# Kernel tuning notes

Hardware: AMD Instinct MI355X
Metric: run time of the kernel (lower is better)

## Reference

```python
import jax, jax.numpy as jnp
import numpy as np

EMB = 2048
H = 16
Q_RANK = 1536
KV_RANK = 512
ROPE_D = 64
NOPE_D = 64
V_D = 128
QK_D = ROPE_D + NOPE_D  # 128
ROPE_BASE = 10000.0
SCALING = 1.0  # query_pre_attn_scalar ** -0.5 with scalar=1.0


def apply_rope(x):
    """torchtune-style interleaved RoPE. x: (B, S, H, D)."""
    S, D = x.shape[1], x.shape[-1]
    theta = 1.0 / (ROPE_BASE ** (jnp.arange(0, D, 2, dtype=jnp.float32) / D))  # (D/2,)
    ang = jnp.arange(S, dtype=jnp.float32)[:, None] * theta[None, :]  # (S, D/2)
    cos = jnp.cos(ang)[None, :, None, :]
    sin = jnp.sin(ang)[None, :, None, :]
    xf = x.astype(jnp.float32).reshape(*x.shape[:-1], D // 2, 2)
    x0, x1 = xf[..., 0], xf[..., 1]
    out = jnp.stack([x0 * cos - x1 * sin, x1 * cos + x0 * sin], axis=-1)
    return out.reshape(x.shape).astype(x.dtype)


def setup_inputs() -> dict:
    key = jax.random.key(0)
    ks = jax.random.split(key, 6)
    s = lambda fan_in: 1.0 / np.sqrt(fan_in)
    return {
        "x": jax.random.normal(ks[0], (2, 2048, EMB), dtype=jnp.float32),
        "q_a_w": jax.random.uniform(ks[1], (Q_RANK, EMB), jnp.float32, -s(EMB), s(EMB)),
        "q_b_w": jax.random.uniform(ks[2], (H * QK_D, Q_RANK), jnp.float32, -s(Q_RANK), s(Q_RANK)),
        "kv_a_w": jax.random.uniform(ks[3], (KV_RANK + ROPE_D, EMB), jnp.float32, -s(EMB), s(EMB)),
        "kv_b_w": jax.random.uniform(ks[4], (H * (NOPE_D + V_D), KV_RANK), jnp.float32, -s(KV_RANK), s(KV_RANK)),
        "o_w": jax.random.uniform(ks[5], (EMB, H * V_D), jnp.float32, -s(H * V_D), s(H * V_D)),
    }


def reference(x, q_a_w, q_b_w, kv_a_w, kv_b_w, o_w):
    B, S, _ = x.shape
    # LoRA-compressed Q projection
    q = (x @ q_a_w.T) @ q_b_w.T  # (B, S, H*QK_D)
    q = q.reshape(B, S, H, QK_D).transpose(0, 2, 1, 3)  # (B, H, S, QK_D)
    q_pass, q_rot = q[..., :NOPE_D], q[..., NOPE_D:]
    # Compressed KV with shared rope key
    ckv = x @ kv_a_w.T  # (B, S, KV_RANK + ROPE_D)
    k_pass_c, k_rot = ckv[..., :KV_RANK], ckv[..., KV_RANK:]
    kvb = (k_pass_c @ kv_b_w.T).reshape(B, S, H, NOPE_D + V_D).transpose(0, 2, 1, 3)
    k_pass, v = kvb[..., :NOPE_D], kvb[..., NOPE_D:]  # (B,H,S,NOPE_D), (B,H,S,V_D)
    # RoPE (applied in (B,S,H,D) layout, as in the original)
    q_rot = apply_rope(q_rot.transpose(0, 2, 1, 3)).transpose(0, 2, 1, 3)
    k_rot = apply_rope(k_rot[:, :, None, :])  # (B, S, 1, ROPE_D), shared across heads
    k_rot = jnp.broadcast_to(k_rot.transpose(0, 2, 1, 3), (B, H, S, ROPE_D))
    query = jnp.concatenate([q_pass, q_rot], axis=-1)  # (B, H, S, QK_D)
    key = jnp.concatenate([k_pass, k_rot], axis=-1)
    # NOTE: original passes attention_mask=None -> no causal mask applied.
    scores = jnp.einsum("bhqd,bhkd->bhqk", query, key) * SCALING
    attn = jax.nn.softmax(scores.astype(jnp.float32), axis=-1).astype(query.dtype)
    out = jnp.einsum("bhqk,bhkd->bhqd", attn, v)  # (B, H, S, V_D)
    out = out.transpose(0, 2, 1, 3).reshape(B, S, H * V_D)
    return out @ o_w.T
```

## Files before the change

### kernel.cpp

```cpp
#include <hip/hip_runtime.h>
#include <stdint.h>

#define EMB 2048
#define NH 16
#define QRANK 1536
#define KVRANK 512
#define ROPED 64
#define NOPED 64
#define VD 128
#define QKD 128
#define SEQ 2048
#define BATCH 2
#define BS 4096
#define BHD 32
#define NCOMB 2112
#define LOG2E 1.4426950408889634f
#define NT (SEQ / 64)

typedef __attribute__((ext_vector_type(4))) float f32x4;
typedef __attribute__((ext_vector_type(8))) short s16x8;
typedef __attribute__((ext_vector_type(4))) short s16x4;
typedef __attribute__((ext_vector_type(2))) unsigned int u32x2;

__device__ __forceinline__ float bf2f(unsigned short u) {
  return __uint_as_float(((unsigned int)u) << 16);
}
__device__ __forceinline__ unsigned short f2bf(float f) {
  unsigned int u = __float_as_uint(f);
  u += 0x7fff + ((u >> 16) & 1);
  return (unsigned short)(u >> 16);
}

__device__ __forceinline__ float vexp2(float x) {
#if __has_builtin(__builtin_amdgcn_exp2f)
  return __builtin_amdgcn_exp2f(x);
#else
  return exp2f(x);
#endif
}

__device__ __forceinline__ unsigned int pk_bf16_trunc(float e0, float e1) {
#if __has_builtin(__builtin_amdgcn_perm)
  return __builtin_amdgcn_perm(__float_as_uint(e1), __float_as_uint(e0), 0x07060302u);
#else
  return (__float_as_uint(e1) & 0xffff0000u) | (__float_as_uint(e0) >> 16);
#endif
}

__device__ __forceinline__ void pl32swap(unsigned int& a, unsigned int& b) {
#if __has_builtin(__builtin_amdgcn_permlane32_swap)
  u32x2 r = __builtin_amdgcn_permlane32_swap(a, b, false, false);
  a = r.x; b = r.y;
#else
  asm("v_permlane32_swap_b32 %0, %1" : "+v"(a), "+v"(b));
#endif
}
__device__ __forceinline__ void pl16swap(unsigned int& a, unsigned int& b) {
#if __has_builtin(__builtin_amdgcn_permlane16_swap)
  u32x2 r = __builtin_amdgcn_permlane16_swap(a, b, false, false);
  a = r.x; b = r.y;
#else
  asm("v_permlane16_swap_b32 %0, %1" : "+v"(a), "+v"(b));
#endif
}

__device__ __forceinline__ void gld_lds16(const unsigned short* g, unsigned short* l) {
  __builtin_amdgcn_global_load_lds((const __attribute__((address_space(1))) void*)g,
                                   (__attribute__((address_space(3))) void*)l,
                                   16, 0, 0);
}

#define N4_X   (BS * EMB / 4)
#define N4_QA  (QRANK * EMB / 4)
#define N4_KVA ((KVRANK + ROPED) * EMB / 4)
#define N4_QB  (NH * QKD * QRANK / 4)
#define N4_KVB (NH * 192 * KVRANK / 4)
#define N4_O   (EMB * NH * VD / 4)
#define N4_TOT (N4_X + N4_QA + N4_KVA + N4_QB + N4_KVB + N4_O)

__global__ void cast_all(const float* __restrict__ x, const float* __restrict__ qa,
                         const float* __restrict__ kva, const float* __restrict__ qb,
                         const float* __restrict__ kvb, const float* __restrict__ ow,
                         unsigned short* __restrict__ Xb, unsigned short* __restrict__ Wcomb,
                         unsigned short* __restrict__ Wqb, unsigned short* __restrict__ Wkvb,
                         unsigned short* __restrict__ Wo) {
  int i = blockIdx.x * blockDim.x + threadIdx.x;
  int stride = gridDim.x * blockDim.x;
  for (; i < N4_TOT; i += stride) {
    const float4* src;
    ushort4* dst;
    int j = i;
    if (j < N4_X) { src = (const float4*)x; dst = (ushort4*)Xb; }
    else if ((j -= N4_X) < N4_QA) { src = (const float4*)qa; dst = (ushort4*)Wcomb; }
    else if ((j -= N4_QA) < N4_KVA) { src = (const float4*)kva; dst = (ushort4*)(Wcomb + (size_t)QRANK * EMB); }
    else if ((j -= N4_KVA) < N4_QB) { src = (const float4*)qb; dst = (ushort4*)Wqb; }
    else if ((j -= N4_QB) < N4_KVB) { src = (const float4*)kvb; dst = (ushort4*)Wkvb; }
    else { j -= N4_KVB; src = (const float4*)ow; dst = (ushort4*)Wo; }
    float4 v = src[j];
    ushort4 o;
    o.x = f2bf(v.x); o.y = f2bf(v.y); o.z = f2bf(v.z); o.w = f2bf(v.w);
    dst[j] = o;
  }
}

template <int OUT_F32>
__global__ __launch_bounds__(256, 3) void gemm_bt(
    const unsigned short* __restrict__ A, int lda,
    const unsigned short* __restrict__ W, int ldw,
    void* __restrict__ C, int M, int N, int K)
{
  __shared__ __align__(16) unsigned short As[128 * 64];
  __shared__ __align__(16) unsigned short Ws[128 * 64];
  const int tid = threadIdx.x;
  const int wave = tid >> 6;
  const int lane = tid & 63;
  const int ln = lane & 15;
  const int quad = lane >> 4;
  const int nwg = gridDim.x;
  const int cpx = nwg >> 3;
  const int swz = (blockIdx.x & 7) * cpx + (blockIdx.x >> 3);
  const int nbx = (N + 127) >> 7;
  const int bm = (swz / nbx) * 128;
  const int bn = (swz % nbx) * 128;
  const int wm = (wave >> 1) * 64;
  const int wn = (wave & 1) * 64;

  f32x4 acc[4][4] = {};

  const int rel8 = lane >> 3;
  const int csw = ((lane & 7) ^ rel8) * 8;

  for (int k0 = 0; k0 < K; k0 += 64) {
#pragma unroll
    for (int it = 0; it < 4; ++it) {
      int rb = wave * 32 + it * 8;
      gld_lds16(A + (size_t)(bm + rb + rel8) * lda + k0 + csw, &As[rb * 64]);
    }
#pragma unroll
    for (int it = 0; it < 4; ++it) {
      int rb = wave * 32 + it * 8;
      int wr = bn + rb + rel8;
      if (wr >= N) wr = N - 1;
      gld_lds16(W + (size_t)wr * ldw + k0 + csw, &Ws[rb * 64]);
    }
    __syncthreads();
#pragma unroll
    for (int kk = 0; kk < 64; kk += 32) {
      s16x8 a[4], b[4];
#pragma unroll
      for (int mt = 0; mt < 4; ++mt)
        a[mt] = *(const s16x8*)&As[(wm + mt * 16 + ln) * 64 + ((kk / 8 + quad) ^ (ln & 7)) * 8];
#pragma unroll
      for (int nt = 0; nt < 4; ++nt)
        b[nt] = *(const s16x8*)&Ws[(wn + nt * 16 + ln) * 64 + ((kk / 8 + quad) ^ (ln & 7)) * 8];
#pragma unroll
      for (int mt = 0; mt < 4; ++mt)
#pragma unroll
        for (int nt = 0; nt < 4; ++nt)
          acc[mt][nt] = __builtin_amdgcn_mfma_f32_16x16x32_bf16(a[mt], b[nt], acc[mt][nt], 0, 0, 0);
    }
    __syncthreads();
  }
#pragma unroll
  for (int mt = 0; mt < 4; ++mt) {
    int row = bm + wm + mt * 16 + quad * 4;
#pragma unroll
    for (int nt = 0; nt < 4; ++nt) {
      int col = bn + wn + nt * 16 + ln;
      if (col < N) {
#pragma unroll
        for (int r = 0; r < 4; ++r) {
          float v = acc[mt][nt][r];
          if (OUT_F32)
            ((float*)C)[(size_t)(row + r) * N + col] = v;
          else
            ((unsigned short*)C)[(size_t)(row + r) * N + col] = f2bf(v);
        }
      }
    }
  }
}

__global__ __launch_bounds__(256, 3) void gemm_q_rope(
    const unsigned short* __restrict__ A, int lda,
    const unsigned short* __restrict__ W, int ldw,
    unsigned short* __restrict__ Qry, int K)
{
  __shared__ __align__(16) unsigned short As[128 * 64];
  __shared__ __align__(16) unsigned short Ws[128 * 64];
  const int tid = threadIdx.x;
  const int wave = tid >> 6;
  const int lane = tid & 63;
  const int ln = lane & 15;
  const int quad = lane >> 4;
  const int nwg = gridDim.x;
  const int cpx = nwg >> 3;
  const int swz = (blockIdx.x & 7) * cpx + (blockIdx.x >> 3);
  const int nbx = (NH * QKD) >> 7;
  const int bm = (swz / nbx) * 128;
  const int bn = (swz % nbx) * 128;
  const int wm = (wave >> 1) * 64;
  const int wn = (wave & 1) * 64;

  f32x4 acc[4][4] = {};
  const int rel8 = lane >> 3;
  const int csw = ((lane & 7) ^ rel8) * 8;

  for (int k0 = 0; k0 < K; k0 += 64) {
#pragma unroll
    for (int it = 0; it < 4; ++it) {
      int rb = wave * 32 + it * 8;
      gld_lds16(A + (size_t)(bm + rb + rel8) * lda + k0 + csw, &As[rb * 64]);
    }
#pragma unroll
    for (int it = 0; it < 4; ++it) {
      int rb = wave * 32 + it * 8;
      gld_lds16(W + (size_t)(bn + rb + rel8) * ldw + k0 + csw, &Ws[rb * 64]);
    }
    __syncthreads();
#pragma unroll
    for (int kk = 0; kk < 64; kk += 32) {
      s16x8 a[4], b[4];
#pragma unroll
      for (int mt = 0; mt < 4; ++mt)
        a[mt] = *(const s16x8*)&As[(wm + mt * 16 + ln) * 64 + ((kk / 8 + quad) ^ (ln & 7)) * 8];
#pragma unroll
      for (int nt = 0; nt < 4; ++nt)
        b[nt] = *(const s16x8*)&Ws[(wn + nt * 16 + ln) * 64 + ((kk / 8 + quad) ^ (ln & 7)) * 8];
#pragma unroll
      for (int mt = 0; mt < 4; ++mt)
#pragma unroll
        for (int nt = 0; nt < 4; ++nt)
          acc[mt][nt] = __builtin_amdgcn_mfma_f32_16x16x32_bf16(a[mt], b[nt], acc[mt][nt], 0, 0, 0);
    }
    __syncthreads();
  }
  const bool odd = (ln & 1);
#pragma unroll
  for (int mt = 0; mt < 4; ++mt) {
    int rowb = bm + wm + mt * 16 + quad * 4;
#pragma unroll
    for (int nt = 0; nt < 4; ++nt) {
      int col = bn + wn + nt * 16 + ln;
      int h = col >> 7, d = col & 127;
#pragma unroll
      for (int r = 0; r < 4; ++r) {
        float v = acc[mt][nt][r];
        float other = __shfl_xor(v, 1);
        int row = rowb + r;
        int b = row >> 11, s = row & 2047;
        float y = v;
        if (d >= NOPED) {
          int i = (d - NOPED) >> 1;
          float theta = exp2f(-(float)i * (13.287712379549449f / 32.f));
          float ang = (float)s * theta;
          float sn, c;
          sincosf(ang, &sn, &c);
          y = v * c + (odd ? other * sn : -other * sn);
        }
        y *= LOG2E;
        Qry[((size_t)(b * NH + h) * SEQ + s) * QKD + d] = f2bf(y);
      }
    }
  }
}

__global__ void prep_kv(const unsigned short* __restrict__ kvb,
                        const unsigned short* __restrict__ cqkv,
                        unsigned short* __restrict__ Key,
                        unsigned short* __restrict__ VT) {
  __shared__ unsigned short vt[64][132];
  __shared__ unsigned short kr[64][64];
  int blk = blockIdx.x;
  int bh = blk >> 5, st = blk & 31;
  int b = bh >> 4, h = bh & 15;
  int s0 = st * 64;
  int tid = threadIdx.x;

  for (int idx = tid; idx < 64 * 32; idx += 256) {
    int sl = idx >> 5, i = idx & 31;
    int s = s0 + sl;
    const unsigned short* rp = cqkv + (size_t)(b * SEQ + s) * NCOMB + QRANK + KVRANK;
    float x0 = bf2f(rp[2 * i]);
    float x1 = bf2f(rp[2 * i + 1]);
    float theta = exp2f(-(float)i * (13.287712379549449f / 32.f));
    float ang = (float)s * theta;
    float sn, c;
    sincosf(ang, &sn, &c);
    kr[sl][2 * i] = f2bf(x0 * c - x1 * sn);
    kr[sl][2 * i + 1] = f2bf(x1 * c + x0 * sn);
  }
  for (int idx = tid; idx < 64 * 16; idx += 256) {
    int sl = idx >> 4, dc = idx & 15;
    s16x8 v = *(const s16x8*)(kvb + (size_t)(b * SEQ + s0 + sl) * (NH * 192) + h * 192 + NOPED + dc * 8);
    *(s16x8*)&vt[sl][dc * 8] = v;
  }
  __syncthreads();
  for (int idx = tid; idx < 64 * 128; idx += 256) {
    int sl = idx >> 7, d = idx & 127;
    unsigned short v;
    if (d < NOPED)
      v = kvb[(size_t)(b * SEQ + s0 + sl) * (NH * 192) + h * 192 + d];
    else
      v = kr[sl][d - NOPED];
    Key[((size_t)bh * SEQ + s0 + sl) * QKD + d] = v;
  }
  for (int idx = tid; idx < 64 * 128; idx += 256) {
    int d = idx >> 6, sl = idx & 63;
    VT[((size_t)bh * VD + d) * SEQ + s0 + sl] = vt[sl][d];
  }
}

__global__ __launch_bounds__(256, 2) void flash_attn(
    const unsigned short* __restrict__ Q,
    const unsigned short* __restrict__ Kt,
    const unsigned short* __restrict__ VT,
    unsigned short* __restrict__ O)
{
  __shared__ __align__(16) unsigned short Ks[2][64 * 128];
  __shared__ __align__(16) unsigned short Vs[3][128 * 64];

  const int tid = threadIdx.x;
  const int wave = tid >> 6;
  const int lane = tid & 63;
  const int ln = lane & 15;
  const int quad = lane >> 4;
  const int bh = blockIdx.x;
  const int q0 = blockIdx.y * 128;
  const int b = bh >> 4, h = bh & 15;

  s16x8 qa[2][4];
#pragma unroll
  for (int mt = 0; mt < 2; ++mt) {
    const unsigned short* qrow = Q + ((size_t)bh * SEQ + q0 + wave * 32 + mt * 16 + ln) * QKD;
#pragma unroll
    for (int kx = 0; kx < 4; ++kx)
      qa[mt][kx] = *(const s16x8*)(qrow + kx * 32 + quad * 8);
  }

  const int krel = lane >> 4, kcch = lane & 15;
  const int vrel8 = lane >> 3;
  const int vc8 = (lane & 7) ^ vrel8;

  auto stage = [&](unsigned short* Kd, unsigned short* Vd, int kt) {
#pragma unroll
    for (int it = 0; it < 4; ++it) {
      int rb = wave * 16 + it * 4;
      int rr = rb + krel;
      int c = kcch ^ (rr & 15);
      gld_lds16(Kt + ((size_t)bh * SEQ + kt * 64 + rr) * QKD + c * 8, Kd + rb * 128);
    }
#pragma unroll
    for (int it = 0; it < 4; ++it) {
      int rb = wave * 32 + it * 8;
      gld_lds16(VT + ((size_t)bh * VD + rb + vrel8) * SEQ + kt * 64 + vc8 * 8, Vd + rb * 64);
    }
  };

  f32x4 o[2][8] = {};
  float l_i[2] = {0.f, 0.f};

  auto sc_init = [&](f32x4 (&sc)[2][4]) {
#pragma unroll
    for (int mt = 0; mt < 2; ++mt)
#pragma unroll
      for (int t = 0; t < 4; ++t)
        sc[mt][t] = (f32x4){-20.f, -20.f, -20.f, -20.f};
  };
  auto qk_kx = [&](int kx, const unsigned short* Kc, f32x4 (&sc)[2][4]) {
    s16x8 ak[4];
#pragma unroll
    for (int t = 0; t < 4; ++t)
      ak[t] = *(const s16x8*)&Kc[(t * 16 + ln) * 128 + ((kx * 4 + quad) ^ ln) * 8];
#pragma unroll
    for (int mt = 0; mt < 2; ++mt)
#pragma unroll
      for (int t = 0; t < 4; ++t)
        sc[mt][t] = __builtin_amdgcn_mfma_f32_16x16x32_bf16(ak[t], qa[mt][kx], sc[mt][t], 0, 0, 0);
  };
  auto sm_mt = [&](int mt, f32x4 (&sc)[2][4], s16x8 (&pfrag)[2][2]) {
    float rs = 0.f;
    unsigned int pw[4][2];
#pragma unroll
    for (int t = 0; t < 4; ++t) {
      float e0 = vexp2(sc[mt][t][0]);
      float e1 = vexp2(sc[mt][t][1]);
      float e2 = vexp2(sc[mt][t][2]);
      float e3 = vexp2(sc[mt][t][3]);
      unsigned int p01 = pk_bf16_trunc(e0, e1);
      unsigned int p23 = pk_bf16_trunc(e2, e3);
      pw[t][0] = p01; pw[t][1] = p23;
      rs += (__uint_as_float(p01 << 16) + __uint_as_float(p01 & 0xffff0000u))
          + (__uint_as_float(p23 << 16) + __uint_as_float(p23 & 0xffff0000u));
    }
    rs += __shfl_xor(rs, 16);
    rs += __shfl_xor(rs, 32);
    l_i[mt] += rs;
#pragma unroll
    for (int W = 0; W < 2; ++W) {
      unsigned int u0 = pw[2 * W][0], v0 = pw[2 * W + 1][0];
      unsigned int u1 = pw[2 * W][1], v1 = pw[2 * W + 1][1];
      pl32swap(u0, v0); pl16swap(u0, v0);
      pl32swap(u1, v1); pl16swap(u1, v1);
      union { unsigned int u[4]; s16x8 v; } fb;
      fb.u[0] = u0;
      fb.u[1] = u1;
      fb.u[2] = v0;
      fb.u[3] = v1;
      pfrag[mt][W] = fb.v;
    }
  };
  auto pv_half = [&](int half, const unsigned short* Vc, s16x8 (&pfrag)[2][2]) {
#pragma unroll
    for (int dd = 0; dd < 4; ++dd) {
      int dt = half * 4 + dd;
      s16x8 av0 = *(const s16x8*)&Vc[(dt * 16 + ln) * 64 + ((quad ^ (ln & 7)) * 8)];
      s16x8 av1 = *(const s16x8*)&Vc[(dt * 16 + ln) * 64 + (((4 + quad) ^ (ln & 7)) * 8)];
#pragma unroll
      for (int mt = 0; mt < 2; ++mt) {
        o[mt][dt] = __builtin_amdgcn_mfma_f32_16x16x32_bf16(av0, pfrag[mt][0], o[mt][dt], 0, 0, 0);
        o[mt][dt] = __builtin_amdgcn_mfma_f32_16x16x32_bf16(av1, pfrag[mt][1], o[mt][dt], 0, 0, 0);
      }
    }
  };

  auto iter = [&](int kt, f32x4 (&scP)[2][4], f32x4 (&scC)[2][4]) {
    asm volatile("s_waitcnt vmcnt(0)" ::: "memory");
    asm volatile("s_barrier" ::: "memory");
    if (kt + 1 < NT)
      stage(Ks[(kt + 1) & 1], Vs[(kt + 1) % 3], kt + 1);
    const unsigned short* Kc = Ks[kt & 1];
    const unsigned short* Vp = Vs[(kt - 1) % 3];
    s16x8 pfrag[2][2];
    __builtin_amdgcn_s_setprio(1);
    sc_init(scC);
    qk_kx(0, Kc, scC);
    sm_mt(0, scP, pfrag);
    qk_kx(1, Kc, scC);
    sm_mt(1, scP, pfrag);
    qk_kx(2, Kc, scC);
    pv_half(0, Vp, pfrag);
    qk_kx(3, Kc, scC);
    pv_half(1, Vp, pfrag);
    __builtin_amdgcn_s_setprio(0);
  };

  f32x4 scA[2][4], scB[2][4];

  stage(Ks[0], Vs[0], 0);
  asm volatile("s_waitcnt vmcnt(0)" ::: "memory");
  asm volatile("s_barrier" ::: "memory");
  stage(Ks[1], Vs[1], 1);
  __builtin_amdgcn_s_setprio(1);
  sc_init(scA);
  qk_kx(0, Ks[0], scA);
  qk_kx(1, Ks[0], scA);
  qk_kx(2, Ks[0], scA);
  qk_kx(3, Ks[0], scA);
  __builtin_amdgcn_s_setprio(0);

  int kt = 1;
#pragma unroll 1
  for (int p = 0; p < 15; ++p, kt += 2) {
    iter(kt, scA, scB);
    iter(kt + 1, scB, scA);
  }
  iter(31, scA, scB);

  {
    s16x8 pfrag[2][2];
    sm_mt(0, scB, pfrag);
    sm_mt(1, scB, pfrag);
    pv_half(0, Vs[1], pfrag);
    pv_half(1, Vs[1], pfrag);
  }

#pragma unroll
  for (int mt = 0; mt < 2; ++mt) {
    float inv = 1.f / l_i[mt];
    int s = q0 + wave * 32 + mt * 16 + ln;
    size_t rowbase = ((size_t)b * SEQ + s) * (NH * VD) + h * VD;
#pragma unroll
    for (int dt = 0; dt < 8; ++dt) {
      ushort4 pk;
      pk.x = f2bf(o[mt][dt][0] * inv);
      pk.y = f2bf(o[mt][dt][1] * inv);
      pk.z = f2bf(o[mt][dt][2] * inv);
      pk.w = f2bf(o[mt][dt][3] * inv);
      *(ushort4*)&O[rowbase + dt * 16 + quad * 4] = pk;
    }
  }
}

extern "C" void kernel_launch(void* const* d_in, const int* in_sizes, int n_in,
                              void* d_out, int out_size, void* d_ws, size_t ws_size,
                              hipStream_t stream) {
  const float* x_f    = (const float*)d_in[0];
  const float* qaw_f  = (const float*)d_in[1];
  const float* qbw_f  = (const float*)d_in[2];
  const float* kvaw_f = (const float*)d_in[3];
  const float* kvbw_f = (const float*)d_in[4];
  const float* ow_f   = (const float*)d_in[5];

  char* ws = (char*)d_ws;
  size_t off = 0;
  auto alloc = [&](size_t n) {
    unsigned short* p = (unsigned short*)(ws + off);
    off = (off + n * 2 + 255) & ~(size_t)255;
    return p;
  };
  unsigned short* Xb    = alloc((size_t)BS * EMB);
  unsigned short* Wcomb = alloc((size_t)NCOMB * EMB);
  unsigned short* Wqb   = alloc((size_t)(NH * QKD) * QRANK);
  unsigned short* Wkvb  = alloc((size_t)(NH * 192) * KVRANK);
  unsigned short* Wo    = alloc((size_t)EMB * (NH * VD));
  unsigned short* CQKV  = alloc((size_t)BS * NCOMB);
  unsigned short* KVB   = alloc((size_t)BS * (NH * 192));
  unsigned short* Qry   = alloc((size_t)BHD * SEQ * QKD);
  unsigned short* Key   = alloc((size_t)BHD * SEQ * QKD);
  unsigned short* Vt    = alloc((size_t)BHD * VD * SEQ);
  unsigned short* AO    = alloc((size_t)BS * (NH * VD));

  cast_all<<<dim3(8192), 256, 0, stream>>>(x_f, qaw_f, kvaw_f, qbw_f, kvbw_f, ow_f,
                                           Xb, Wcomb, Wqb, Wkvb, Wo);

  gemm_bt<0><<<dim3(((NCOMB + 127) / 128) * (BS / 128)), 256, 0, stream>>>(
      Xb, EMB, Wcomb, EMB, CQKV, BS, NCOMB, EMB);
  gemm_q_rope<<<dim3(((NH * QKD) / 128) * (BS / 128)), 256, 0, stream>>>(
      CQKV, NCOMB, Wqb, QRANK, Qry, QRANK);
  gemm_bt<0><<<dim3(((NH * 192) / 128) * (BS / 128)), 256, 0, stream>>>(
      CQKV + QRANK, NCOMB, Wkvb, KVRANK, KVB, BS, NH * 192, KVRANK);

  prep_kv<<<dim3(BHD * (SEQ / 64)), 256, 0, stream>>>(KVB, CQKV, Key, Vt);

  flash_attn<<<dim3(BHD, SEQ / 128), 256, 0, stream>>>(Qry, Key, Vt, AO);

  gemm_bt<1><<<dim3((EMB / 128) * (BS / 128)), 256, 0, stream>>>(
      AO, NH * VD, Wo, NH * VD, d_out, BS, EMB, NH * VD);
}
```

Before: 354.0 us.

## Overlap weight casts with first GEMM and merge Q/KV up-projection GEMMs

Splits the cast kernel so only x and the first-stage weights are cast up front. The remaining weight casts run as extra blocks inside the first GEMM launch, and the Q-rope and KV-b GEMMs are merged into one launch with block-range dispatch. This reduces kernel count and fills idle CUs during smaller GEMMs. It also vectorizes the Key write in prep_kv to 16-byte stores. The risk is that heterogeneous blocks in one launch can schedule unevenly, and cast blocks may compete with GEMM blocks for bandwidth.

```diff
diff --git a/kernel.cpp b/kernel.cpp
--- a/kernel.cpp
+++ b/kernel.cpp
@@ -76,24 +76,132 @@
 #define N4_QB  (NH * QKD * QRANK / 4)
 #define N4_KVB (NH * 192 * KVRANK / 4)
 #define N4_O   (EMB * NH * VD / 4)
-#define N4_TOT (N4_X + N4_QA + N4_KVA + N4_QB + N4_KVB + N4_O)
-
-__global__ void cast_all(const float* __restrict__ x, const float* __restrict__ qa,
-                         const float* __restrict__ kva, const float* __restrict__ qb,
-                         const float* __restrict__ kvb, const float* __restrict__ ow,
-                         unsigned short* __restrict__ Xb, unsigned short* __restrict__ Wcomb,
-                         unsigned short* __restrict__ Wqb, unsigned short* __restrict__ Wkvb,
-                         unsigned short* __restrict__ Wo) {
+#define N4A_TOT (N4_X + N4_QA + N4_KVA)
+#define N4B_TOT (N4_QB + N4_KVB + N4_O)
+
+__global__ void cast_a(const float* __restrict__ x, const float* __restrict__ qa,
+                       const float* __restrict__ kva,
+                       unsigned short* __restrict__ Xb, unsigned short* __restrict__ Wcomb) {
   int i = blockIdx.x * blockDim.x + threadIdx.x;
   int stride = gridDim.x * blockDim.x;
-  for (; i < N4_TOT; i += stride) {
+  for (; i < N4A_TOT; i += stride) {
     const float4* src;
     ushort4* dst;
     int j = i;
     if (j < N4_X) { src = (const float4*)x; dst = (ushort4*)Xb; }
     else if ((j -= N4_X) < N4_QA) { src = (const float4*)qa; dst = (ushort4*)Wcomb; }
-    else if ((j -= N4_QA) < N4_KVA) { src = (const float4*)kva; dst = (ushort4*)(Wcomb + (size_t)QRANK * EMB); }
-    else if ((j -= N4_KVA) < N4_QB) { src = (const float4*)qb; dst = (ushort4*)Wqb; }
+    else { j -= N4_QA; src = (const float4*)kva; dst = (ushort4*)(Wcomb + (size_t)QRANK * EMB); }
+    float4 v = src[j];
+    ushort4 o;
+    o.x = f2bf(v.x); o.y = f2bf(v.y); o.z = f2bf(v.z); o.w = f2bf(v.w);
+    dst[j] = o;
+  }
+}
+
+__device__ __forceinline__ void gemm_core(
+    unsigned short* As, unsigned short* Ws,
+    const unsigned short* __restrict__ A, int lda,
+    const unsigned short* __restrict__ W, int ldw,
+    int N, int K, int bm, int bn, bool clamp, f32x4 (&acc)[4][4]) {
+  const int tid = threadIdx.x;
+  const int wave = tid >> 6;
+  const int lane = tid & 63;
+  const int ln = lane & 15;
+  const int quad = lane >> 4;
+  const int wm = (wave >> 1) * 64;
+  const int wn = (wave & 1) * 64;
+  const int rel8 = lane >> 3;
+  const int csw = ((lane & 7) ^ rel8) * 8;
+
+  for (int k0 = 0; k0 < K; k0 += 64) {
+#pragma unroll
+    for (int it = 0; it < 4; ++it) {
+      int rb = wave * 32 + it * 8;
+      gld_lds16(A + (size_t)(bm + rb + rel8) * lda + k0 + csw, &As[rb * 64]);
+    }
+#pragma unroll
+    for (int it = 0; it < 4; ++it) {
+      int rb = wave * 32 + it * 8;
+      int wr = bn + rb + rel8;
+      if (clamp && wr >= N) wr = N - 1;
+      gld_lds16(W + (size_t)wr * ldw + k0 + csw, &Ws[rb * 64]);
+    }
+    __syncthreads();
+#pragma unroll
+    for (int kk = 0; kk < 64; kk += 32) {
+      s16x8 a[4], b[4];
+#pragma unroll
+      for (int mt = 0; mt < 4; ++mt)
+        a[mt] = *(const s16x8*)&As[(wm + mt * 16 + ln) * 64 + ((kk / 8 + quad) ^ (ln & 7)) * 8];
+#pragma unroll
+      for (int nt = 0; nt < 4; ++nt)
+        b[nt] = *(const s16x8*)&Ws[(wn + nt * 16 + ln) * 64 + ((kk / 8 + quad) ^ (ln & 7)) * 8];
+#pragma unroll
+      for (int mt = 0; mt < 4; ++mt)
+#pragma unroll
+        for (int nt = 0; nt < 4; ++nt)
+          acc[mt][nt] = __builtin_amdgcn_mfma_f32_16x16x32_bf16(a[mt], b[nt], acc[mt][nt], 0, 0, 0);
+    }
+    __syncthreads();
+  }
+}
+
+__device__ __forceinline__ void gemm_store(f32x4 (&acc)[4][4], void* C, int N,
+                                           int bm, int bn, int out_f32) {
+  const int tid = threadIdx.x;
+  const int wave = tid >> 6;
+  const int lane = tid & 63;
+  const int ln = lane & 15;
+  const int quad = lane >> 4;
+  const int wm = (wave >> 1) * 64;
+  const int wn = (wave & 1) * 64;
+#pragma unroll
+  for (int mt = 0; mt < 4; ++mt) {
+    int row = bm + wm + mt * 16 + quad * 4;
+#pragma unroll
+    for (int nt = 0; nt < 4; ++nt) {
+      int col = bn + wn + nt * 16 + ln;
+      if (col < N) {
+#pragma unroll
+        for (int r = 0; r < 4; ++r) {
+          float v = acc[mt][nt][r];
+          if (out_f32)
+            ((float*)C)[(size_t)(row + r) * N + col] = v;
+          else
+            ((unsigned short*)C)[(size_t)(row + r) * N + col] = f2bf(v);
+        }
+      }
+    }
+  }
+}
+
+#define G1_BLOCKS 544
+#define G1CAST_GRID 2048
+__global__ __launch_bounds__(256, 3) void gemm_a_castb(
+    const unsigned short* __restrict__ Xb, const unsigned short* __restrict__ Wcomb,
+    unsigned short* __restrict__ CQKV,
+    const float* __restrict__ qb, const float* __restrict__ kvb, const float* __restrict__ ow,
+    unsigned short* __restrict__ Wqb, unsigned short* __restrict__ Wkvb,
+    unsigned short* __restrict__ Wo) {
+  __shared__ __align__(16) unsigned short As[128 * 64];
+  __shared__ __align__(16) unsigned short Ws[128 * 64];
+  const int bid = blockIdx.x;
+  if (bid < G1_BLOCKS) {
+    const int swz = (bid & 7) * (G1_BLOCKS / 8) + (bid >> 3);
+    const int bm = (swz / 17) * 128;
+    const int bn = (swz % 17) * 128;
+    f32x4 acc[4][4] = {};
+    gemm_core(As, Ws, Xb, EMB, Wcomb, EMB, NCOMB, EMB, bm, bn, true, acc);
+    gemm_store(acc, CQKV, NCOMB, bm, bn, 0);
+    return;
+  }
+  int i = (bid - G1_BLOCKS) * 256 + threadIdx.x;
+  const int stride = (G1CAST_GRID - G1_BLOCKS) * 256;
+  for (; i < N4B_TOT; i += stride) {
+    const float4* src;
+    ushort4* dst;
+    int j = i;
+    if (j < N4_QB) { src = (const float4*)qb; dst = (ushort4*)Wqb; }
     else if ((j -= N4_QB) < N4_KVB) { src = (const float4*)kvb; dst = (ushort4*)Wkvb; }
     else { j -= N4_KVB; src = (const float4*)ow; dst = (ushort4*)Wo; }
     float4 v = src[j];
@@ -103,138 +211,38 @@
   }
 }
 
-template <int OUT_F32>
-__global__ __launch_bounds__(256, 3) void gemm_bt(
-    const unsigned short* __restrict__ A, int lda,
-    const unsigned short* __restrict__ W, int ldw,
-    void* __restrict__ C, int M, int N, int K)
-{
+#define GQ_BLOCKS 512
+#define GKV_BLOCKS 768
+__global__ __launch_bounds__(256, 3) void gemm_qkv(
+    const unsigned short* __restrict__ CQKV,
+    const unsigned short* __restrict__ Wqb, const unsigned short* __restrict__ Wkvb,
+    unsigned short* __restrict__ Qry, unsigned short* __restrict__ KVB) {
   __shared__ __align__(16) unsigned short As[128 * 64];
   __shared__ __align__(16) unsigned short Ws[128 * 64];
+  const int bid = blockIdx.x;
+  if (bid >= GQ_BLOCKS) {
+    const int b2 = bid - GQ_BLOCKS;
+    const int swz = (b2 & 7) * (GKV_BLOCKS / 8) + (b2 >> 3);
+    const int bm = (swz / 24) * 128;
+    const int bn = (swz % 24) * 128;
+    f32x4 acc[4][4] = {};
+    gemm_core(As, Ws, CQKV + QRANK, NCOMB, Wkvb, KVRANK, NH * 192, KVRANK, bm, bn, false, acc);
+    gemm_store(acc, KVB, NH * 192, bm, bn, 0);
+    return;
+  }
+  const int swz = (bid & 7) * (GQ_BLOCKS / 8) + (bid >> 3);
+  const int bm = (swz / 16) * 128;
+  const int bn = (swz % 16) * 128;
+  f32x4 acc[4][4] = {};
+  gemm_core(As, Ws, CQKV, NCOMB, Wqb, QRANK, NH * QKD, QRANK, bm, bn, false, acc);
+
   const int tid = threadIdx.x;
   const int wave = tid >> 6;
   const int lane = tid & 63;
   const int ln = lane & 15;
   const int quad = lane >> 4;
-  const int nwg = gridDim.x;
-  const int cpx = nwg >> 3;
-  const int swz = (blockIdx.x & 7) * cpx + (blockIdx.x >> 3);
-  const int nbx = (N + 127) >> 7;
-  const int bm = (swz / nbx) * 128;
-  const int bn = (swz % nbx) * 128;
   const int wm = (wave >> 1) * 64;
   const int wn = (wave & 1) * 64;
-
-  f32x4 acc[4][4] = {};
-
-  const int rel8 = lane >> 3;
-  const int csw = ((lane & 7) ^ rel8) * 8;
-
-  for (int k0 = 0; k0 < K; k0 += 64) {
-#pragma unroll
-    for (int it = 0; it < 4; ++it) {
-      int rb = wave * 32 + it * 8;
-      gld_lds16(A + (size_t)(bm + rb + rel8) * lda + k0 + csw, &As[rb * 64]);
-    }
-#pragma unroll
-    for (int it = 0; it < 4; ++it) {
-      int rb = wave * 32 + it * 8;
-      int wr = bn + rb + rel8;
-      if (wr >= N) wr = N - 1;
-      gld_lds16(W + (size_t)wr * ldw + k0 + csw, &Ws[rb * 64]);
-    }
-    __syncthreads();
-#pragma unroll
-    for (int kk = 0; kk < 64; kk += 32) {
-      s16x8 a[4], b[4];
-#pragma unroll
-      for (int mt = 0; mt < 4; ++mt)
-        a[mt] = *(const s16x8*)&As[(wm + mt * 16 + ln) * 64 + ((kk / 8 + quad) ^ (ln & 7)) * 8];
-#pragma unroll
-      for (int nt = 0; nt < 4; ++nt)
-        b[nt] = *(const s16x8*)&Ws[(wn + nt * 16 + ln) * 64 + ((kk / 8 + quad) ^ (ln & 7)) * 8];
-#pragma unroll
-      for (int mt = 0; mt < 4; ++mt)
-#pragma unroll
-        for (int nt = 0; nt < 4; ++nt)
-          acc[mt][nt] = __builtin_amdgcn_mfma_f32_16x16x32_bf16(a[mt], b[nt], acc[mt][nt], 0, 0, 0);
-    }
-    __syncthreads();
-  }
-#pragma unroll
-  for (int mt = 0; mt < 4; ++mt) {
-    int row = bm + wm + mt * 16 + quad * 4;
-#pragma unroll
-    for (int nt = 0; nt < 4; ++nt) {
-      int col = bn + wn + nt * 16 + ln;
-      if (col < N) {
-#pragma unroll
-        for (int r = 0; r < 4; ++r) {
-          float v = acc[mt][nt][r];
-          if (OUT_F32)
-            ((float*)C)[(size_t)(row + r) * N + col] = v;
-          else
-            ((unsigned short*)C)[(size_t)(row + r) * N + col] = f2bf(v);
-        }
-      }
-    }
-  }
-}
-
-__global__ __launch_bounds__(256, 3) void gemm_q_rope(
-    const unsigned short* __restrict__ A, int lda,
-    const unsigned short* __restrict__ W, int ldw,
-    unsigned short* __restrict__ Qry, int K)
-{
-  __shared__ __align__(16) unsigned short As[128 * 64];
-  __shared__ __align__(16) unsigned short Ws[128 * 64];
-  const int tid = threadIdx.x;
-  const int wave = tid >> 6;
-  const int lane = tid & 63;
-  const int ln = lane & 15;
-  const int quad = lane >> 4;
-  const int nwg = gridDim.x;
-  const int cpx = nwg >> 3;
-  const int swz = (blockIdx.x & 7) * cpx + (blockIdx.x >> 3);
-  const int nbx = (NH * QKD) >> 7;
-  const int bm = (swz / nbx) * 128;
-  const int bn = (swz % nbx) * 128;
-  const int wm = (wave >> 1) * 64;
-  const int wn = (wave & 1) * 64;
-
-  f32x4 acc[4][4] = {};
-  const int rel8 = lane >> 3;
-  const int csw = ((lane & 7) ^ rel8) * 8;
-
-  for (int k0 = 0; k0 < K; k0 += 64) {
-#pragma unroll
-    for (int it = 0; it < 4; ++it) {
-      int rb = wave * 32 + it * 8;
-      gld_lds16(A + (size_t)(bm + rb + rel8) * lda + k0 + csw, &As[rb * 64]);
-    }
-#pragma unroll
-    for (int it = 0; it < 4; ++it) {
-      int rb = wave * 32 + it * 8;
-      gld_lds16(W + (size_t)(bn + rb + rel8) * ldw + k0 + csw, &Ws[rb * 64]);
-    }
-    __syncthreads();
-#pragma unroll
-    for (int kk = 0; kk < 64; kk += 32) {
-      s16x8 a[4], b[4];
-#pragma unroll
-      for (int mt = 0; mt < 4; ++mt)
-        a[mt] = *(const s16x8*)&As[(wm + mt * 16 + ln) * 64 + ((kk / 8 + quad) ^ (ln & 7)) * 8];
-#pragma unroll
-      for (int nt = 0; nt < 4; ++nt)
-        b[nt] = *(const s16x8*)&Ws[(wn + nt * 16 + ln) * 64 + ((kk / 8 + quad) ^ (ln & 7)) * 8];
-#pragma unroll
-      for (int mt = 0; mt < 4; ++mt)
-#pragma unroll
-        for (int nt = 0; nt < 4; ++nt)
-          acc[mt][nt] = __builtin_amdgcn_mfma_f32_16x16x32_bf16(a[mt], b[nt], acc[mt][nt], 0, 0, 0);
-    }
-    __syncthreads();
-  }
   const bool odd = (ln & 1);
 #pragma unroll
   for (int mt = 0; mt < 4; ++mt) {
@@ -296,14 +304,14 @@
     *(s16x8*)&vt[sl][dc * 8] = v;
   }
   __syncthreads();
-  for (int idx = tid; idx < 64 * 128; idx += 256) {
-    int sl = idx >> 7, d = idx & 127;
-    unsigned short v;
-    if (d < NOPED)
-      v = kvb[(size_t)(b * SEQ + s0 + sl) * (NH * 192) + h * 192 + d];
+  for (int idx = tid; idx < 64 * 16; idx += 256) {
+    int sl = idx >> 4, dc = idx & 15;
+    s16x8 v;
+    if (dc < 8)
+      v = *(const s16x8*)(kvb + (size_t)(b * SEQ + s0 + sl) * (NH * 192) + h * 192 + dc * 8);
     else
-      v = kr[sl][d - NOPED];
-    Key[((size_t)bh * SEQ + s0 + sl) * QKD + d] = v;
+      v = *(const s16x8*)&kr[sl][(dc - 8) * 8];
+    *(s16x8*)&Key[((size_t)bh * SEQ + s0 + sl) * QKD + dc * 8] = v;
   }
   for (int idx = tid; idx < 64 * 128; idx += 256) {
     int d = idx >> 6, sl = idx & 63;
@@ -492,6 +500,23 @@
   }
 }
 
+__global__ __launch_bounds__(256, 3) void gemm_out(
+    const unsigned short* __restrict__ A, int lda,
+    const unsigned short* __restrict__ W, int ldw,
+    float* __restrict__ C, int N, int K) {
+  __shared__ __align__(16) unsigned short As[128 * 64];
+  __shared__ __align__(16) unsigned short Ws[128 * 64];
+  const int nwg = gridDim.x;
+  const int cpx = nwg >> 3;
+  const int swz = (blockIdx.x & 7) * cpx + (blockIdx.x >> 3);
+  const int nbx = N >> 7;
+  const int bm = (swz / nbx) * 128;
+  const int bn = (swz % nbx) * 128;
+  f32x4 acc[4][4] = {};
+  gemm_core(As, Ws, A, lda, W, ldw, N, K, bm, bn, false, acc);
+  gemm_store(acc, C, N, bm, bn, 1);
+}
+
 extern "C" void kernel_launch(void* const* d_in, const int* in_sizes, int n_in,
                               void* d_out, int out_size, void* d_ws, size_t ws_size,
                               hipStream_t stream) {
@@ -521,20 +546,18 @@
   unsigned short* Vt    = alloc((size_t)BHD * VD * SEQ);
   unsigned short* AO    = alloc((size_t)BS * (NH * VD));
 
-  cast_all<<<dim3(8192), 256, 0, stream>>>(x_f, qaw_f, kvaw_f, qbw_f, kvbw_f, ow_f,
-                                           Xb, Wcomb, Wqb, Wkvb, Wo);
-
-  gemm_bt<0><<<dim3(((NCOMB + 127) / 128) * (BS / 128)), 256, 0, stream>>>(
-      Xb, EMB, Wcomb, EMB, CQKV, BS, NCOMB, EMB);
-  gemm_q_rope<<<dim3(((NH * QKD) / 128) * (BS / 128)), 256, 0, stream>>>(
-      CQKV, NCOMB, Wqb, QRANK, Qry, QRANK);
-  gemm_bt<0><<<dim3(((NH * 192) / 128) * (BS / 128)), 256, 0, stream>>>(
-      CQKV + QRANK, NCOMB, Wkvb, KVRANK, KVB, BS, NH * 192, KVRANK);
+  cast_a<<<dim3(4096), 256, 0, stream>>>(x_f, qaw_f, kvaw_f, Xb, Wcomb);
+
+  gemm_a_castb<<<dim3(G1CAST_GRID), 256, 0, stream>>>(
+      Xb, Wcomb, CQKV, qbw_f, kvbw_f, ow_f, Wqb, Wkvb, Wo);
+
+  gemm_qkv<<<dim3(GQ_BLOCKS + GKV_BLOCKS), 256, 0, stream>>>(
+      CQKV, Wqb, Wkvb, Qry, KVB);
 
   prep_kv<<<dim3(BHD * (SEQ / 64)), 256, 0, stream>>>(KVB, CQKV, Key, Vt);
 
   flash_attn<<<dim3(BHD, SEQ / 128), 256, 0, stream>>>(Qry, Key, Vt, AO);
 
-  gemm_bt<1><<<dim3((EMB / 128) * (BS / 128)), 256, 0, stream>>>(
-      AO, NH * VD, Wo, NH * VD, d_out, BS, EMB, NH * VD);
-}
+  gemm_out<<<dim3((EMB / 128) * (BS / 128)), 256, 0, stream>>>(
+      AO, NH * VD, Wo, NH * VD, (float*)d_out, EMB, NH * VD);
+}
```

Result: no change. 356.3 us (median of 3 runs) (+0.7%).
